# Kernel tuning notes

Measured on AMD Instinct MI355X. Metric: run time of the kernel, lower is better.

Reference implementation:

```python
import jax, jax.numpy as jnp
import numpy as np

STATE_DIM, SKILL_DIM = 256, 64
HID = 1024
LAT = 128
B = 4096
TEMP = 1.0


def _init_linear(key, fan_in, fan_out):
    # torch nn.Linear default init: U(-1/sqrt(fan_in), 1/sqrt(fan_in))
    kw, kb = jax.random.split(key)
    bound = 1.0 / np.sqrt(fan_in)
    W = jax.random.uniform(kw, (fan_in, fan_out), jnp.float32, -bound, bound)
    b = jax.random.uniform(kb, (fan_out,), jnp.float32, -bound, bound)
    return W, b


def setup_inputs() -> dict:
    key = jax.random.key(0)
    ks = jax.random.split(key, 8)
    x = jax.random.normal(ks[0], (B, STATE_DIM), jnp.float32)
    y = jax.random.normal(ks[1], (B, SKILL_DIM), jnp.float32)
    sW1, sb1 = _init_linear(ks[2], STATE_DIM, HID)
    sW2, sb2 = _init_linear(ks[3], HID, HID)
    sW3, sb3 = _init_linear(ks[4], HID, LAT)
    kW1, kb1 = _init_linear(ks[5], SKILL_DIM, HID)
    kW2, kb2 = _init_linear(ks[6], HID, HID)
    kW3, kb3 = _init_linear(ks[7], HID, LAT)
    return {
        "x": x, "y": y,
        "sW1": sW1, "sb1": sb1, "sW2": sW2, "sb2": sb2, "sW3": sW3, "sb3": sb3,
        "kW1": kW1, "kb1": kb1, "kW2": kW2, "kb2": kb2, "kW3": kW3, "kb3": kb3,
    }


def _mlp(x, W1, b1, W2, b2, W3, b3):
    h = jax.nn.relu(x @ W1 + b1)
    h = jax.nn.relu(h @ W2 + b2)
    return h @ W3 + b3


def _l2norm(v, eps=1e-12):
    # matches F.normalize(dim=-1): v / max(||v||, eps)
    n = jnp.sqrt(jnp.sum(v * v, axis=-1, keepdims=True))
    return v / jnp.maximum(n, eps)


def reference(x, y, sW1, sb1, sW2, sb2, sW3, sb3, kW1, kb1, kW2, kb2, kW3, kb3):
    zx = _l2norm(_mlp(x, sW1, sb1, sW2, sb2, sW3, sb3))  # [B, LAT]
    zy = _l2norm(_mlp(y, kW1, kb1, kW2, kb2, kW3, kb3))  # [B, LAT]
    # sum(x[:,None,:]*y[None,:,:], -1) == zx @ zy.T (same math, no BxBxD blowup)
    scores = jnp.einsum('id,jd->ij', zx, zy) / TEMP       # [B, B]
    # InfoNCE lower bound: log(B) - CE(scores, arange(B)), reduction='none'
    logp = jax.nn.log_softmax(scores, axis=-1)
    nll = jnp.diagonal(logp)                               # = -CE per row
    mi = jnp.log(jnp.float32(scores.shape[0])) + nll       # [B]
    return scores, mi
```

## Files before the change

### kernel.cpp

```cpp
#include <hip/hip_runtime.h>
#include <hip/hip_bf16.h>
#include <math.h>

typedef __bf16 v8bf __attribute__((ext_vector_type(8)));
typedef float  v4f  __attribute__((ext_vector_type(4)));

#define GPTR(p) ((const __attribute__((address_space(1))) void*)(p))
#define LPTR(p) ((__attribute__((address_space(3))) void*)(p))

struct PrepArgs {
    const float* x; const float* y;
    __hip_bfloat16* xb; __hip_bfloat16* yb;
    int nx4, ntot4;
    const float* wsrc[6];
    __hip_bfloat16* wdst[6];
    int K[6], N[6];
};

__global__ __launch_bounds__(256)
void prep_k(PrepArgs a) {
    const int tid = threadIdx.x, bx = blockIdx.x, z = blockIdx.z;
    if (z == 0) {
        int i = bx * 256 + tid;
        if (i >= a.ntot4) return;
        const float* src; __hip_bfloat16* dst; int j;
        if (i < a.nx4) { src = a.x; dst = a.xb; j = i; }
        else           { src = a.y; dst = a.yb; j = i - a.nx4; }
        float4 v = ((const float4*)src)[j];
        __hip_bfloat16 h[4] = {__float2bfloat16(v.x), __float2bfloat16(v.y),
                               __float2bfloat16(v.z), __float2bfloat16(v.w)};
        ((short4*)dst)[j] = *(short4*)h;
        return;
    }
    int w = z - 1;
    int K = a.K[w], N = a.N[w];
    int tn = N >> 5;
    int tt = (K >> 5) * tn;
    if (bx >= tt) return;
    int kt = (bx / tn) * 32, nt = (bx % tn) * 32;
    __shared__ float t[32][33];
    int tx = tid & 31, ty = tid >> 5;
    const float* W = a.wsrc[w];
    __hip_bfloat16* Wt = a.wdst[w];
#pragma unroll
    for (int i = 0; i < 4; ++i)
        t[ty + i * 8][tx] = W[(size_t)(kt + ty + i * 8) * N + nt + tx];
    __syncthreads();
#pragma unroll
    for (int i = 0; i < 4; ++i)
        Wt[(size_t)(nt + ty + i * 8) * K + kt + tx] =
            __float2bfloat16(t[tx][ty + i * 8]);
}

__device__ __forceinline__ void stage128(
    const __hip_bfloat16* __restrict__ A, const __hip_bfloat16* __restrict__ Bt,
    int lda, int ldb, int bm, int bn, int k0, int wid, int crow, int ccol,
    __hip_bfloat16* As, __hip_bfloat16* Bs) {
#pragma unroll
    for (int i = 0; i < 4; ++i) {
        int c = wid * 4 + i;
        __builtin_amdgcn_global_load_lds(
            GPTR(A + (size_t)(bm + c * 8 + crow) * lda + k0 + ccol),
            LPTR(As + c * 512), 16, 0, 0);
        __builtin_amdgcn_global_load_lds(
            GPTR(Bt + (size_t)(bn + c * 8 + crow) * ldb + k0 + ccol),
            LPTR(Bs + c * 512), 16, 0, 0);
    }
}

__device__ __forceinline__ void compute128(
    const __hip_bfloat16* As, const __hip_bfloat16* Bs,
    int lane, int wr, int wc, v4f acc[4][4]) {
#pragma unroll
    for (int kk = 0; kk < 64; kk += 32) {
        v8bf a[4], b[4];
#pragma unroll
        for (int i = 0; i < 4; ++i) {
            a[i] = *(const v8bf*)&As[(wr * 64 + i * 16 + (lane & 15)) * 64 + kk + (lane >> 4) * 8];
            b[i] = *(const v8bf*)&Bs[(wc * 64 + i * 16 + (lane & 15)) * 64 + kk + (lane >> 4) * 8];
        }
#pragma unroll
        for (int i = 0; i < 4; ++i)
#pragma unroll
            for (int j = 0; j < 4; ++j)
                acc[i][j] = __builtin_amdgcn_mfma_f32_16x16x32_bf16(
                    a[i], b[j], acc[i][j], 0, 0, 0);
    }
}

struct MlpArgs {
    const __hip_bfloat16* A[2];
    const __hip_bfloat16* B[2];
    const float* bias[2];
    __hip_bfloat16* C[2];
    int K[2];
};

__global__ __launch_bounds__(256)
void gemm_mlp_k(MlpArgs args) {
    __shared__ __align__(16) __hip_bfloat16 As0[128 * 64], As1[128 * 64];
    __shared__ __align__(16) __hip_bfloat16 Bs0[128 * 64], Bs1[128 * 64];

    const int bid = blockIdx.x;
    const int wg  = (bid & 7) * 64 + (bid >> 3);
    const int z   = wg >> 8;
    const int rem = wg & 255;
    const int bm  = (rem >> 3) * 128;
    const int bn  = (rem & 7) * 128;

    const int tid = threadIdx.x, wid = tid >> 6, lane = tid & 63;
    const int wr = wid >> 1, wc = wid & 1;
    const int crow = lane >> 3, ccol = (lane & 7) * 8;
    const __hip_bfloat16* A  = args.A[z];
    const __hip_bfloat16* Bt = args.B[z];
    const int K = args.K[z];
    const int nt = K >> 6;

    v4f acc[4][4] = {};
    stage128(A, Bt, K, K, bm, bn, 0, wid, crow, ccol, As0, Bs0);
    __syncthreads();
    for (int t = 0; t < nt; ++t) {
        const bool odd = t & 1;
        if (t + 1 < nt)
            stage128(A, Bt, K, K, bm, bn, (t + 1) * 64, wid, crow, ccol,
                     odd ? As0 : As1, odd ? Bs0 : Bs1);
        compute128(odd ? As1 : As0, odd ? Bs1 : Bs0, lane, wr, wc, acc);
        __syncthreads();
    }

    const float* bias = args.bias[z];
    __hip_bfloat16* C = args.C[z];
#pragma unroll
    for (int i = 0; i < 4; ++i) {
        int rowb = bm + wr * 64 + i * 16 + (lane >> 4) * 4;
#pragma unroll
        for (int j = 0; j < 4; ++j) {
            int col = bn + wc * 64 + j * 16 + (lane & 15);
            float bv = bias[col];
#pragma unroll
            for (int r = 0; r < 4; ++r) {
                float v = fmaxf(acc[i][j][r] + bv, 0.f);
                C[(size_t)(rowb + r) * 1024 + col] = __float2bfloat16(v);
            }
        }
    }
}

__global__ __launch_bounds__(256)
void gemm_l3norm_k(const __hip_bfloat16* __restrict__ As_g0,
                   const __hip_bfloat16* __restrict__ As_g1,
                   const __hip_bfloat16* __restrict__ Bt0,
                   const __hip_bfloat16* __restrict__ Bt1,
                   const float* __restrict__ sb3, const float* __restrict__ kb3,
                   __hip_bfloat16* __restrict__ zxb,
                   __hip_bfloat16* __restrict__ zyb) {
    __shared__ __align__(16) __hip_bfloat16 As[2][32 * 64];
    __shared__ __align__(16) __hip_bfloat16 Bs[2][128 * 64];
    __shared__ float red[4][32];
    const int bid = blockIdx.x;
    const int wg  = (bid & 7) * 32 + (bid >> 3);
    const int z   = wg >> 7;
    const int bm  = (wg & 127) * 32;

    const __hip_bfloat16* A  = z ? As_g1 : As_g0;
    const __hip_bfloat16* Bt = z ? Bt1 : Bt0;
    const float* bias = z ? kb3 : sb3;
    __hip_bfloat16* zout = z ? zyb : zxb;

    const int tid = threadIdx.x, wid = tid >> 6, lane = tid & 63;
    const int crow = lane >> 3, ccol = (lane & 7) * 8;

    auto stage = [&](int buf, int k0) {
        __builtin_amdgcn_global_load_lds(
            GPTR(A + (size_t)(bm + wid * 8 + crow) * 1024 + k0 + ccol),
            LPTR(&As[buf][wid * 512]), 16, 0, 0);
#pragma unroll
        for (int i = 0; i < 4; ++i) {
            int c = wid * 4 + i;
            __builtin_amdgcn_global_load_lds(
                GPTR(Bt + (size_t)(c * 8 + crow) * 1024 + k0 + ccol),
                LPTR(&Bs[buf][c * 512]), 16, 0, 0);
        }
    };
    auto compute = [&](int buf, v4f acc[2][2]) {
#pragma unroll
        for (int kk = 0; kk < 64; kk += 32) {
            v8bf a[2], b[2];
#pragma unroll
            for (int i = 0; i < 2; ++i)
                a[i] = *(const v8bf*)&As[buf][(i * 16 + (lane & 15)) * 64 + kk + (lane >> 4) * 8];
#pragma unroll
            for (int j = 0; j < 2; ++j)
                b[j] = *(const v8bf*)&Bs[buf][(wid * 32 + j * 16 + (lane & 15)) * 64 + kk + (lane >> 4) * 8];
#pragma unroll
            for (int i = 0; i < 2; ++i)
#pragma unroll
                for (int j = 0; j < 2; ++j)
                    acc[i][j] = __builtin_amdgcn_mfma_f32_16x16x32_bf16(
                        a[i], b[j], acc[i][j], 0, 0, 0);
        }
    };

    v4f acc[2][2] = {};
    stage(0, 0);
    __syncthreads();
    for (int t = 0; t < 16; ++t) {
        const int cur = t & 1;
        if (t + 1 < 16) stage(cur ^ 1, (t + 1) * 64);
        compute(cur, acc);
        __syncthreads();
    }

    float val[2][2][4];
    float ssq[2][4];
#pragma unroll
    for (int i = 0; i < 2; ++i)
#pragma unroll
        for (int r = 0; r < 4; ++r) ssq[i][r] = 0.f;
#pragma unroll
    for (int i = 0; i < 2; ++i)
#pragma unroll
        for (int j = 0; j < 2; ++j) {
            int col = wid * 32 + j * 16 + (lane & 15);
            float bv = bias[col];
#pragma unroll
            for (int r = 0; r < 4; ++r) {
                float v = acc[i][j][r] + bv;
                val[i][j][r] = v;
                ssq[i][r] += v * v;
            }
        }
#pragma unroll
    for (int i = 0; i < 2; ++i)
#pragma unroll
        for (int r = 0; r < 4; ++r) {
#pragma unroll
            for (int m = 1; m < 16; m <<= 1)
                ssq[i][r] += __shfl_xor(ssq[i][r], m, 64);
            if ((lane & 15) == 0)
                red[wid][i * 16 + (lane >> 4) * 4 + r] = ssq[i][r];
        }
    __syncthreads();
#pragma unroll
    for (int i = 0; i < 2; ++i)
#pragma unroll
        for (int r = 0; r < 4; ++r) {
            int row = i * 16 + (lane >> 4) * 4 + r;
            float ss = red[0][row] + red[1][row] + red[2][row] + red[3][row];
            float inv = 1.0f / fmaxf(sqrtf(ss), 1e-12f);
#pragma unroll
            for (int j = 0; j < 2; ++j) {
                int col = wid * 32 + j * 16 + (lane & 15);
                zout[(size_t)(bm + row) * 128 + col] =
                    __float2bfloat16(val[i][j][r] * inv);
            }
        }
}

__global__ __launch_bounds__(256)
void gemm_scores_k(const __hip_bfloat16* __restrict__ zxb,
                   const __hip_bfloat16* __restrict__ zyb,
                   float* __restrict__ out, float* __restrict__ esum) {
    __shared__ __align__(16) __hip_bfloat16 As[128 * 64], Bs[128 * 64];
    __shared__ float rowsum[2][128];
    const int tid = threadIdx.x, wid = tid >> 6, lane = tid & 63;
    const int wr = wid >> 1, wc = wid & 1;
    const int bm = blockIdx.x * 128, bn = blockIdx.y * 128;
    const int crow = lane >> 3, ccol = (lane & 7) * 8;
    v4f acc[4][4] = {};
#pragma unroll
    for (int t = 0; t < 2; ++t) {
        stage128(zxb, zyb, 128, 128, bm, bn, t * 64, wid, crow, ccol, As, Bs);
        __syncthreads();
        compute128(As, Bs, lane, wr, wc, acc);
        __syncthreads();
    }
#pragma unroll
    for (int i = 0; i < 4; ++i) {
        int rowb = bm + wr * 64 + i * 16 + (lane >> 4) * 4;
#pragma unroll
        for (int r = 0; r < 4; ++r) {
            float s = 0.f;
#pragma unroll
            for (int j = 0; j < 4; ++j) {
                int col = bn + wc * 64 + j * 16 + (lane & 15);
                float v = acc[i][j][r];
                __builtin_nontemporal_store(v, &out[(size_t)(rowb + r) * 4096 + col]);
                s += __expf(v - 1.0f);
            }
#pragma unroll
            for (int m = 1; m < 16; m <<= 1) s += __shfl_xor(s, m, 64);
            if ((lane & 15) == 0)
                rowsum[wc][wr * 64 + i * 16 + (lane >> 4) * 4 + r] = s;
        }
    }
    __syncthreads();
    if (tid < 128)
        esum[(size_t)(bm + tid) * 32 + blockIdx.y] =
            rowsum[0][tid] + rowsum[1][tid];
}

__global__ __launch_bounds__(256)
void mi_k(const float* __restrict__ esum, const float* __restrict__ scores,
          float* __restrict__ mi) {
    int row = blockIdx.x * 256 + threadIdx.x;
    const float4* p = (const float4*)&esum[(size_t)row * 32];
    float s = 0.f;
#pragma unroll
    for (int i = 0; i < 8; ++i) { float4 v = p[i]; s += v.x + v.y + v.z + v.w; }
    float diag = scores[(size_t)row * 4096 + row];
    mi[row] = 8.317766166719343f + diag - 1.0f - logf(s);
}

extern "C" void kernel_launch(void* const* d_in, const int* in_sizes, int n_in,
                              void* d_out, int out_size, void* d_ws, size_t ws_size,
                              hipStream_t stream) {
    const float* x   = (const float*)d_in[0];
    const float* y   = (const float*)d_in[1];
    const float* sW1 = (const float*)d_in[2];
    const float* sb1 = (const float*)d_in[3];
    const float* sW2 = (const float*)d_in[4];
    const float* sb2 = (const float*)d_in[5];
    const float* sW3 = (const float*)d_in[6];
    const float* sb3 = (const float*)d_in[7];
    const float* kW1 = (const float*)d_in[8];
    const float* kb1 = (const float*)d_in[9];
    const float* kW2 = (const float*)d_in[10];
    const float* kb2 = (const float*)d_in[11];
    const float* kW3 = (const float*)d_in[12];
    const float* kb3 = (const float*)d_in[13];

    float* out = (float*)d_out;
    float* mi  = out + (size_t)4096 * 4096;

    char* ws = (char*)d_ws;
    auto alloc = [&](size_t bytes) {
        char* p = ws;
        ws += (bytes + 255) & ~(size_t)255;
        return p;
    };
    __hip_bfloat16* xb   = (__hip_bfloat16*)alloc((size_t)4096 * 256 * 2);
    __hip_bfloat16* yb   = (__hip_bfloat16*)alloc((size_t)4096 * 64 * 2);
    __hip_bfloat16* sW1t = (__hip_bfloat16*)alloc((size_t)1024 * 256 * 2);
    __hip_bfloat16* sW2t = (__hip_bfloat16*)alloc((size_t)1024 * 1024 * 2);
    __hip_bfloat16* sW3t = (__hip_bfloat16*)alloc((size_t)128 * 1024 * 2);
    __hip_bfloat16* kW1t = (__hip_bfloat16*)alloc((size_t)1024 * 64 * 2);
    __hip_bfloat16* kW2t = (__hip_bfloat16*)alloc((size_t)1024 * 1024 * 2);
    __hip_bfloat16* kW3t = (__hip_bfloat16*)alloc((size_t)128 * 1024 * 2);
    __hip_bfloat16* h1s  = (__hip_bfloat16*)alloc((size_t)4096 * 1024 * 2);
    __hip_bfloat16* h1k  = (__hip_bfloat16*)alloc((size_t)4096 * 1024 * 2);
    __hip_bfloat16* h2s  = (__hip_bfloat16*)alloc((size_t)4096 * 1024 * 2);
    __hip_bfloat16* h2k  = (__hip_bfloat16*)alloc((size_t)4096 * 1024 * 2);
    float*          es   = (float*)alloc((size_t)4096 * 32 * 4);
    __hip_bfloat16* zxb  = (__hip_bfloat16*)alloc((size_t)4096 * 128 * 2);
    __hip_bfloat16* zyb  = (__hip_bfloat16*)alloc((size_t)4096 * 128 * 2);

    PrepArgs pa;
    pa.x = x; pa.y = y; pa.xb = xb; pa.yb = yb;
    pa.nx4 = 4096 * 256 / 4;
    pa.ntot4 = pa.nx4 + 4096 * 64 / 4;
    pa.wsrc[0] = sW1; pa.wdst[0] = sW1t; pa.K[0] = 256;  pa.N[0] = 1024;
    pa.wsrc[1] = sW2; pa.wdst[1] = sW2t; pa.K[1] = 1024; pa.N[1] = 1024;
    pa.wsrc[2] = sW3; pa.wdst[2] = sW3t; pa.K[2] = 1024; pa.N[2] = 128;
    pa.wsrc[3] = kW1; pa.wdst[3] = kW1t; pa.K[3] = 64;   pa.N[3] = 1024;
    pa.wsrc[4] = kW2; pa.wdst[4] = kW2t; pa.K[4] = 1024; pa.N[4] = 1024;
    pa.wsrc[5] = kW3; pa.wdst[5] = kW3t; pa.K[5] = 1024; pa.N[5] = 128;
    prep_k<<<dim3(1280, 1, 7), 256, 0, stream>>>(pa);

    MlpArgs l1;
    l1.A[0] = xb;  l1.B[0] = sW1t; l1.bias[0] = sb1; l1.C[0] = h1s; l1.K[0] = 256;
    l1.A[1] = yb;  l1.B[1] = kW1t; l1.bias[1] = kb1; l1.C[1] = h1k; l1.K[1] = 64;
    gemm_mlp_k<<<512, 256, 0, stream>>>(l1);

    MlpArgs l2;
    l2.A[0] = h1s; l2.B[0] = sW2t; l2.bias[0] = sb2; l2.C[0] = h2s; l2.K[0] = 1024;
    l2.A[1] = h1k; l2.B[1] = kW2t; l2.bias[1] = kb2; l2.C[1] = h2k; l2.K[1] = 1024;
    gemm_mlp_k<<<512, 256, 0, stream>>>(l2);

    gemm_l3norm_k<<<256, 256, 0, stream>>>(
        h2s, h2k, sW3t, kW3t, sb3, kb3, zxb, zyb);

    gemm_scores_k<<<dim3(32, 32), 256, 0, stream>>>(zxb, zyb, out, es);

    mi_k<<<16, 256, 0, stream>>>(es, out, mi);
}
```

Before: 90.03 us.

## Overlap W2/W3 weight transposes with layer-1 GEMM and halve L3 row tile

Splits the weight-prep kernel so only the layer-1 weights and inputs are converted up front. The large W2/W3 transposes run as extra blocks inside the layer-1 GEMM launch, so their memory traffic can overlap the small layer-1 matmul. Separately, the layer-3+normalize kernel now uses 16-row tiles instead of 32, doubling its grid to 512 blocks for better CU occupancy, at the cost of re-reading the W3 tile more often. The merged kernel's LDS footprint now includes the transpose buffer.

```diff
diff --git a/kernel.cpp b/kernel.cpp
--- a/kernel.cpp
+++ b/kernel.cpp
@@ -8,20 +8,34 @@
 #define GPTR(p) ((const __attribute__((address_space(1))) void*)(p))
 #define LPTR(p) ((__attribute__((address_space(3))) void*)(p))
 
-struct PrepArgs {
+__device__ __forceinline__ void transpose_tile(
+    const float* __restrict__ W, __hip_bfloat16* __restrict__ Wt,
+    int K, int N, int kt, int nt, int tid, float (*t)[33]) {
+    int tx = tid & 31, ty = tid >> 5;
+#pragma unroll
+    for (int i = 0; i < 4; ++i)
+        t[ty + i * 8][tx] = W[(size_t)(kt + ty + i * 8) * N + nt + tx];
+    __syncthreads();
+#pragma unroll
+    for (int i = 0; i < 4; ++i)
+        Wt[(size_t)(nt + ty + i * 8) * K + kt + tx] =
+            __float2bfloat16(t[tx][ty + i * 8]);
+}
+
+struct Prep1Args {
     const float* x; const float* y;
     __hip_bfloat16* xb; __hip_bfloat16* yb;
     int nx4, ntot4;
-    const float* wsrc[6];
-    __hip_bfloat16* wdst[6];
-    int K[6], N[6];
+    const float* sW1; __hip_bfloat16* sW1t;
+    const float* kW1; __hip_bfloat16* kW1t;
 };
 
 __global__ __launch_bounds__(256)
-void prep_k(PrepArgs a) {
-    const int tid = threadIdx.x, bx = blockIdx.x, z = blockIdx.z;
-    if (z == 0) {
-        int i = bx * 256 + tid;
+void prep1_k(Prep1Args a) {
+    __shared__ float t[32][33];
+    const int tid = threadIdx.x, bid = blockIdx.x;
+    if (bid < 1280) {
+        int i = bid * 256 + tid;
         if (i >= a.ntot4) return;
         const float* src; __hip_bfloat16* dst; int j;
         if (i < a.nx4) { src = a.x; dst = a.xb; j = i; }
@@ -32,24 +46,13 @@
         ((short4*)dst)[j] = *(short4*)h;
         return;
     }
-    int w = z - 1;
-    int K = a.K[w], N = a.N[w];
-    int tn = N >> 5;
-    int tt = (K >> 5) * tn;
-    if (bx >= tt) return;
-    int kt = (bx / tn) * 32, nt = (bx % tn) * 32;
-    __shared__ float t[32][33];
-    int tx = tid & 31, ty = tid >> 5;
-    const float* W = a.wsrc[w];
-    __hip_bfloat16* Wt = a.wdst[w];
-#pragma unroll
-    for (int i = 0; i < 4; ++i)
-        t[ty + i * 8][tx] = W[(size_t)(kt + ty + i * 8) * N + nt + tx];
-    __syncthreads();
-#pragma unroll
-    for (int i = 0; i < 4; ++i)
-        Wt[(size_t)(nt + ty + i * 8) * K + kt + tx] =
-            __float2bfloat16(t[tx][ty + i * 8]);
+    int ti = bid - 1280;
+    if (ti < 256)
+        transpose_tile(a.sW1, a.sW1t, 256, 1024,
+                       (ti >> 5) * 32, (ti & 31) * 32, tid, t);
+    else
+        transpose_tile(a.kW1, a.kW1t, 64, 1024,
+                       ((ti - 256) >> 5) * 32, ((ti - 256) & 31) * 32, tid, t);
 }
 
 __device__ __forceinline__ void stage128(
@@ -88,32 +91,17 @@
     }
 }
 
-struct MlpArgs {
-    const __hip_bfloat16* A[2];
-    const __hip_bfloat16* B[2];
-    const float* bias[2];
-    __hip_bfloat16* C[2];
-    int K[2];
-};
-
-__global__ __launch_bounds__(256)
-void gemm_mlp_k(MlpArgs args) {
-    __shared__ __align__(16) __hip_bfloat16 As0[128 * 64], As1[128 * 64];
-    __shared__ __align__(16) __hip_bfloat16 Bs0[128 * 64], Bs1[128 * 64];
-
-    const int bid = blockIdx.x;
-    const int wg  = (bid & 7) * 64 + (bid >> 3);
-    const int z   = wg >> 8;
+__device__ __forceinline__ void gemm_body(
+    const __hip_bfloat16* A, const __hip_bfloat16* Bt, const float* bias,
+    __hip_bfloat16* C, int K, int wg,
+    __hip_bfloat16* As0, __hip_bfloat16* As1,
+    __hip_bfloat16* Bs0, __hip_bfloat16* Bs1) {
     const int rem = wg & 255;
     const int bm  = (rem >> 3) * 128;
     const int bn  = (rem & 7) * 128;
-
     const int tid = threadIdx.x, wid = tid >> 6, lane = tid & 63;
     const int wr = wid >> 1, wc = wid & 1;
     const int crow = lane >> 3, ccol = (lane & 7) * 8;
-    const __hip_bfloat16* A  = args.A[z];
-    const __hip_bfloat16* Bt = args.B[z];
-    const int K = args.K[z];
     const int nt = K >> 6;
 
     v4f acc[4][4] = {};
@@ -127,9 +115,6 @@
         compute128(odd ? As1 : As0, odd ? Bs1 : Bs0, lane, wr, wc, acc);
         __syncthreads();
     }
-
-    const float* bias = args.bias[z];
-    __hip_bfloat16* C = args.C[z];
 #pragma unroll
     for (int i = 0; i < 4; ++i) {
         int rowb = bm + wr * 64 + i * 16 + (lane >> 4) * 4;
@@ -144,6 +129,69 @@
             }
         }
     }
+}
+
+struct L1Args {
+    const __hip_bfloat16* A[2];
+    const __hip_bfloat16* B[2];
+    const float* bias[2];
+    __hip_bfloat16* C[2];
+    int K[2];
+    const float* sW2; __hip_bfloat16* sW2t;
+    const float* kW2; __hip_bfloat16* kW2t;
+    const float* sW3; __hip_bfloat16* sW3t;
+    const float* kW3; __hip_bfloat16* kW3t;
+};
+
+__global__ __launch_bounds__(256)
+void l1_merged_k(L1Args args) {
+    __shared__ __align__(16) __hip_bfloat16 As0[128 * 64], As1[128 * 64];
+    __shared__ __align__(16) __hip_bfloat16 Bs0[128 * 64], Bs1[128 * 64];
+    __shared__ float t[32][33];
+    const int bid = blockIdx.x, tid = threadIdx.x;
+    if (bid < 512) {
+        const int wg = (bid & 7) * 64 + (bid >> 3);
+        const int z  = wg >> 8;
+        gemm_body(args.A[z], args.B[z], args.bias[z], args.C[z], args.K[z],
+                  wg, As0, As1, Bs0, Bs1);
+        return;
+    }
+    int ti = bid - 512;
+    if (ti < 1024)
+        transpose_tile(args.sW2, args.sW2t, 1024, 1024,
+                       (ti >> 5) * 32, (ti & 31) * 32, tid, t);
+    else if (ti < 2048) {
+        ti -= 1024;
+        transpose_tile(args.kW2, args.kW2t, 1024, 1024,
+                       (ti >> 5) * 32, (ti & 31) * 32, tid, t);
+    } else if (ti < 2176) {
+        ti -= 2048;
+        transpose_tile(args.sW3, args.sW3t, 1024, 128,
+                       (ti >> 2) * 32, (ti & 3) * 32, tid, t);
+    } else {
+        ti -= 2176;
+        transpose_tile(args.kW3, args.kW3t, 1024, 128,
+                       (ti >> 2) * 32, (ti & 3) * 32, tid, t);
+    }
+}
+
+struct MlpArgs {
+    const __hip_bfloat16* A[2];
+    const __hip_bfloat16* B[2];
+    const float* bias[2];
+    __hip_bfloat16* C[2];
+    int K[2];
+};
+
+__global__ __launch_bounds__(256)
+void gemm_mlp_k(MlpArgs args) {
+    __shared__ __align__(16) __hip_bfloat16 As0[128 * 64], As1[128 * 64];
+    __shared__ __align__(16) __hip_bfloat16 Bs0[128 * 64], Bs1[128 * 64];
+    const int bid = blockIdx.x;
+    const int wg  = (bid & 7) * 64 + (bid >> 3);
+    const int z   = wg >> 8;
+    gemm_body(args.A[z], args.B[z], args.bias[z], args.C[z], args.K[z],
+              wg, As0, As1, Bs0, Bs1);
 }
 
 __global__ __launch_bounds__(256)
@@ -154,13 +202,13 @@
                    const float* __restrict__ sb3, const float* __restrict__ kb3,
                    __hip_bfloat16* __restrict__ zxb,
                    __hip_bfloat16* __restrict__ zyb) {
-    __shared__ __align__(16) __hip_bfloat16 As[2][32 * 64];
+    __shared__ __align__(16) __hip_bfloat16 As[2][16 * 64];
     __shared__ __align__(16) __hip_bfloat16 Bs[2][128 * 64];
-    __shared__ float red[4][32];
+    __shared__ float red[4][16];
     const int bid = blockIdx.x;
-    const int wg  = (bid & 7) * 32 + (bid >> 3);
-    const int z   = wg >> 7;
-    const int bm  = (wg & 127) * 32;
+    const int wg  = (bid & 7) * 64 + (bid >> 3);
+    const int z   = wg >> 8;
+    const int bm  = (wg & 255) * 16;
 
     const __hip_bfloat16* A  = z ? As_g1 : As_g0;
     const __hip_bfloat16* Bt = z ? Bt1 : Bt0;
@@ -171,9 +219,10 @@
     const int crow = lane >> 3, ccol = (lane & 7) * 8;
 
     auto stage = [&](int buf, int k0) {
-        __builtin_amdgcn_global_load_lds(
-            GPTR(A + (size_t)(bm + wid * 8 + crow) * 1024 + k0 + ccol),
-            LPTR(&As[buf][wid * 512]), 16, 0, 0);
+        if (wid < 2)
+            __builtin_amdgcn_global_load_lds(
+                GPTR(A + (size_t)(bm + wid * 8 + crow) * 1024 + k0 + ccol),
+                LPTR(&As[buf][wid * 512]), 16, 0, 0);
 #pragma unroll
         for (int i = 0; i < 4; ++i) {
             int c = wid * 4 + i;
@@ -182,26 +231,22 @@
                 LPTR(&Bs[buf][c * 512]), 16, 0, 0);
         }
     };
-    auto compute = [&](int buf, v4f acc[2][2]) {
+    auto compute = [&](int buf, v4f acc[2]) {
 #pragma unroll
         for (int kk = 0; kk < 64; kk += 32) {
-            v8bf a[2], b[2];
-#pragma unroll
-            for (int i = 0; i < 2; ++i)
-                a[i] = *(const v8bf*)&As[buf][(i * 16 + (lane & 15)) * 64 + kk + (lane >> 4) * 8];
+            v8bf a, b[2];
+            a = *(const v8bf*)&As[buf][((lane & 15)) * 64 + kk + (lane >> 4) * 8];
 #pragma unroll
             for (int j = 0; j < 2; ++j)
                 b[j] = *(const v8bf*)&Bs[buf][(wid * 32 + j * 16 + (lane & 15)) * 64 + kk + (lane >> 4) * 8];
 #pragma unroll
-            for (int i = 0; i < 2; ++i)
-#pragma unroll
-                for (int j = 0; j < 2; ++j)
-                    acc[i][j] = __builtin_amdgcn_mfma_f32_16x16x32_bf16(
-                        a[i], b[j], acc[i][j], 0, 0, 0);
+            for (int j = 0; j < 2; ++j)
+                acc[j] = __builtin_amdgcn_mfma_f32_16x16x32_bf16(
+                    a, b[j], acc[j], 0, 0, 0);
         }
     };
 
-    v4f acc[2][2] = {};
+    v4f acc[2] = {};
     stage(0, 0);
     __syncthreads();
     for (int t = 0; t < 16; ++t) {
@@ -211,50 +256,42 @@
         __syncthreads();
     }
 
-    float val[2][2][4];
-    float ssq[2][4];
-#pragma unroll
-    for (int i = 0; i < 2; ++i)
-#pragma unroll
-        for (int r = 0; r < 4; ++r) ssq[i][r] = 0.f;
-#pragma unroll
-    for (int i = 0; i < 2; ++i)
+    float val[2][4];
+    float ssq[4];
+#pragma unroll
+    for (int r = 0; r < 4; ++r) ssq[r] = 0.f;
+#pragma unroll
+    for (int j = 0; j < 2; ++j) {
+        int col = wid * 32 + j * 16 + (lane & 15);
+        float bv = bias[col];
+#pragma unroll
+        for (int r = 0; r < 4; ++r) {
+            float v = acc[j][r] + bv;
+            val[j][r] = v;
+            ssq[r] += v * v;
+        }
+    }
+#pragma unroll
+    for (int r = 0; r < 4; ++r) {
+#pragma unroll
+        for (int m = 1; m < 16; m <<= 1)
+            ssq[r] += __shfl_xor(ssq[r], m, 64);
+        if ((lane & 15) == 0)
+            red[wid][(lane >> 4) * 4 + r] = ssq[r];
+    }
+    __syncthreads();
+#pragma unroll
+    for (int r = 0; r < 4; ++r) {
+        int row = (lane >> 4) * 4 + r;
+        float ss = red[0][row] + red[1][row] + red[2][row] + red[3][row];
+        float inv = 1.0f / fmaxf(sqrtf(ss), 1e-12f);
 #pragma unroll
         for (int j = 0; j < 2; ++j) {
             int col = wid * 32 + j * 16 + (lane & 15);
-            float bv = bias[col];
-#pragma unroll
-            for (int r = 0; r < 4; ++r) {
-                float v = acc[i][j][r] + bv;
-                val[i][j][r] = v;
-                ssq[i][r] += v * v;
-            }
-        }
-#pragma unroll
-    for (int i = 0; i < 2; ++i)
-#pragma unroll
-        for (int r = 0; r < 4; ++r) {
-#pragma unroll
-            for (int m = 1; m < 16; m <<= 1)
-                ssq[i][r] += __shfl_xor(ssq[i][r], m, 64);
-            if ((lane & 15) == 0)
-                red[wid][i * 16 + (lane >> 4) * 4 + r] = ssq[i][r];
-        }
-    __syncthreads();
-#pragma unroll
-    for (int i = 0; i < 2; ++i)
-#pragma unroll
-        for (int r = 0; r < 4; ++r) {
-            int row = i * 16 + (lane >> 4) * 4 + r;
-            float ss = red[0][row] + red[1][row] + red[2][row] + red[3][row];
-            float inv = 1.0f / fmaxf(sqrtf(ss), 1e-12f);
-#pragma unroll
-            for (int j = 0; j < 2; ++j) {
-                int col = wid * 32 + j * 16 + (lane & 15);
-                zout[(size_t)(bm + row) * 128 + col] =
-                    __float2bfloat16(val[i][j][r] * inv);
-            }
-        }
+            zout[(size_t)(bm + row) * 128 + col] =
+                __float2bfloat16(val[j][r] * inv);
+        }
+    }
 }
 
 __global__ __launch_bounds__(256)
@@ -355,29 +392,29 @@
     __hip_bfloat16* zxb  = (__hip_bfloat16*)alloc((size_t)4096 * 128 * 2);
     __hip_bfloat16* zyb  = (__hip_bfloat16*)alloc((size_t)4096 * 128 * 2);
 
-    PrepArgs pa;
-    pa.x = x; pa.y = y; pa.xb = xb; pa.yb = yb;
-    pa.nx4 = 4096 * 256 / 4;
-    pa.ntot4 = pa.nx4 + 4096 * 64 / 4;
-    pa.wsrc[0] = sW1; pa.wdst[0] = sW1t; pa.K[0] = 256;  pa.N[0] = 1024;
-    pa.wsrc[1] = sW2; pa.wdst[1] = sW2t; pa.K[1] = 1024; pa.N[1] = 1024;
-    pa.wsrc[2] = sW3; pa.wdst[2] = sW3t; pa.K[2] = 1024; pa.N[2] = 128;
-    pa.wsrc[3] = kW1; pa.wdst[3] = kW1t; pa.K[3] = 64;   pa.N[3] = 1024;
-    pa.wsrc[4] = kW2; pa.wdst[4] = kW2t; pa.K[4] = 1024; pa.N[4] = 1024;
-    pa.wsrc[5] = kW3; pa.wdst[5] = kW3t; pa.K[5] = 1024; pa.N[5] = 128;
-    prep_k<<<dim3(1280, 1, 7), 256, 0, stream>>>(pa);
-
-    MlpArgs l1;
+    Prep1Args p1;
+    p1.x = x; p1.y = y; p1.xb = xb; p1.yb = yb;
+    p1.nx4 = 4096 * 256 / 4;
+    p1.ntot4 = p1.nx4 + 4096 * 64 / 4;
+    p1.sW1 = sW1; p1.sW1t = sW1t;
+    p1.kW1 = kW1; p1.kW1t = kW1t;
+    prep1_k<<<1280 + 256 + 64, 256, 0, stream>>>(p1);
+
+    L1Args l1;
     l1.A[0] = xb;  l1.B[0] = sW1t; l1.bias[0] = sb1; l1.C[0] = h1s; l1.K[0] = 256;
     l1.A[1] = yb;  l1.B[1] = kW1t; l1.bias[1] = kb1; l1.C[1] = h1k; l1.K[1] = 64;
-    gemm_mlp_k<<<512, 256, 0, stream>>>(l1);
+    l1.sW2 = sW2; l1.sW2t = sW2t;
+    l1.kW2 = kW2; l1.kW2t = kW2t;
+    l1.sW3 = sW3; l1.sW3t = sW3t;
+    l1.kW3 = kW3; l1.kW3t = kW3t;
+    l1_merged_k<<<512 + 2304, 256, 0, stream>>>(l1);
 
     MlpArgs l2;
     l2.A[0] = h1s; l2.B[0] = sW2t; l2.bias[0] = sb2; l2.C[0] = h2s; l2.K[0] = 1024;
     l2.A[1] = h1k; l2.B[1] = kW2t; l2.bias[1] = kb2; l2.C[1] = h2k; l2.K[1] = 1024;
     gemm_mlp_k<<<512, 256, 0, stream>>>(l2);
 
-    gemm_l3norm_k<<<256, 256, 0, stream>>>(
+    gemm_l3norm_k<<<512, 256, 0, stream>>>(
         h2s, h2k, sW3t, kW3t, sb3, kb3, zxb, zyb);
 
     gemm_scores_k<<<dim3(32, 32), 256, 0, stream>>>(zxb, zyb, out, es);
```

Result: no change. 91.18 us (+1.3%).
